# Optimization experiments

Hardware: AMD Instinct MI355X
Metric: run time of the kernel (lower is better)

Reference implementation:

```python
import jax, jax.numpy as jnp
import numpy as np

KH = KW = 3  # fixed: distortion() generates a 9-tap (3x3) offset grid


def make_offset(h, w, dilation=1.0, skydome=True):
    """Faithful numpy port of DistortionConvLayer.distortion -> [1,h,w,9,2] (last dim = [x_off, y_off])."""
    pi = np.pi
    unit_w = 2.0 * pi / w
    unit_h = pi / (2.0 * h) if skydome else pi / h
    rho = np.tan(unit_w) * dilation
    v = np.array([0.0, 1.0, 0.0])
    r_grid = np.array([[1, -1], [1, 0], [1, 1], [0, -1], [0, 0], [0, 1], [-1, -1], [-1, 0], [-1, 1]], dtype=np.float64)
    xc = int(w * 0.5)
    theta = (xc - 0.5 * w) * unit_w
    y = np.arange(h, dtype=np.float64)
    phi = (h - y) * unit_h if skydome else (h * 0.5 - y) * unit_h  # [h]
    p_u = np.stack([np.cos(phi) * np.cos(theta), np.sin(phi), np.cos(phi) * np.sin(theta)], axis=-1)  # [h,3]
    t_x = np.cross(np.broadcast_to(v, p_u.shape), p_u)  # [h,3]
    t_y = np.cross(p_u, t_x)                            # [h,3]
    # r_sphere: [h,9,3]
    r_sphere = rho * (r_grid[None, :, 0, None] * t_x[:, None, :] + r_grid[None, :, 1, None] * t_y[:, None, :])
    p_ur = p_u[:, None, :] + r_sphere  # [h,9,3]
    ux, uy, uz = p_ur[..., 0], p_ur[..., 1], p_ur[..., 2]
    base = np.arctan2(uz, ux)
    theta_r = np.where(ux > 0, base,
               np.where(ux < 0, np.where(uz >= 0, base + pi, base - pi),
                np.where(uz > 0, pi * 0.5, -pi * 0.5)))
    phi_r = np.arcsin(uy)
    x_r = (theta_r / pi + 1.0) * 0.5 * w
    y_r = (1.0 - 2.0 * phi_r / pi) * h if skydome else (0.5 - phi_r / pi) * h
    k = np.stack([x_r, y_r], axis=-1)          # [h,9,2], entries [x, y] (as in original)
    off = k - k[:, 4:5, :]                      # subtract center tap
    off = np.broadcast_to(off[:, None, :, :], (h, w, 9, 2))  # tile over width
    return off[None].astype(np.float32)         # [1,h,w,9,2]


def setup_inputs() -> dict:
    key = jax.random.key(0)
    k1, k2 = jax.random.split(key)
    B, H, W, C, F = 4, 128, 256, 64, 128
    inputs = jax.random.normal(k1, (B, H, W, C), dtype=jnp.float32)
    fan_in = KH * KW * C
    kernel = jax.random.normal(k2, (fan_in, F), dtype=jnp.float32) * (1.0 / np.sqrt(fan_in))
    bias = jnp.zeros((F,), dtype=jnp.float32)
    return {"inputs": inputs, "kernel": kernel, "bias": bias}


def reference(inputs, kernel, bias):
    B, H, W, C = inputs.shape
    F = kernel.shape[1]
    off = jnp.asarray(make_offset(H, W))  # [1,H,W,9,2], static constant
    # 'same' padding for 3x3, stride 1, dilation 1 -> pad 1 on each side
    xp = jnp.pad(inputs, ((0, 0), (1, 1), (1, 1), (0, 0)))
    in_h, in_w = H + 2, W + 2
    # base conv sampling coordinates (extract_patches order: tap k -> dy=k//3, dx=k%3)
    dy = jnp.repeat(jnp.arange(KH), KW).astype(jnp.float32)  # [9]
    dx = jnp.tile(jnp.arange(KW), KH).astype(jnp.float32)    # [9]
    base_y = jnp.arange(H, dtype=jnp.float32)[None, :, None, None] + dy[None, None, None, :]  # [1,H,1,9]
    base_x = jnp.arange(W, dtype=jnp.float32)[None, None, :, None] + dx[None, None, None, :]  # [1,1,W,9]
    # NOTE: faithful to original: channel 0 of offset (x_r diffs) is added to y, channel 1 to x
    y = base_y + off[..., 0]  # [1,H,W,9]
    x = base_x + off[..., 1]
    y = jnp.clip(y, 0.0, in_h - 1)
    x = jnp.where(x < 0, x + in_w, x)
    x = jnp.where(x > in_w - 1, x - in_w, x)
    y0 = jnp.floor(y).astype(jnp.int32)
    x0 = jnp.floor(x).astype(jnp.int32)
    y1, x1 = y0 + 1, x0 + 1
    y0 = jnp.clip(y0, 0, in_h - 1); y1 = jnp.clip(y1, 0, in_h - 1)
    x0 = jnp.clip(x0, 0, in_w - 1); x1 = jnp.clip(x1, 0, in_w - 1)
    bidx = jnp.arange(B)[:, None, None, None]  # [B,1,1,1], broadcasts against [1,H,W,9]
    gather = lambda yi, xi: xp[bidx, yi, xi]   # -> [B,H,W,9,C]
    p0 = gather(y0, x0); p1 = gather(y0, x1); p2 = gather(y1, x0); p3 = gather(y1, x1)
    y0f, y1f = y0.astype(jnp.float32), y1.astype(jnp.float32)
    x0f, x1f = x0.astype(jnp.float32), x1.astype(jnp.float32)
    w0 = ((y1f - y) * (x1f - x))[..., None]
    w1 = ((y1f - y) * (x - x0f))[..., None]
    w2 = ((y - y0f) * (x1f - x))[..., None]
    w3 = ((y - y0f) * (x - x0f))[..., None]
    pixels = w0 * p0 + w1 * p1 + w2 * p2 + w3 * p3  # [B,H,W,9,C]
    pixels = pixels.reshape(B, H * W, KH * KW * C)
    out = pixels @ kernel + bias                    # [B,HW,F]
    return jax.nn.relu(out.reshape(B, H, W, F))
```

## Files before the change

### kernel.cpp

```cpp
#include <hip/hip_runtime.h>
#include <math.h>

#define Bb 4
#define Hh 128
#define Ww 256
#define Cc 64
#define Ff 128
#define INH 130
#define INW 258

#define WSLOT 72
#define WCOLS 68

typedef __attribute__((ext_vector_type(8))) __bf16 bf16x8;
typedef __attribute__((ext_vector_type(4))) float floatx4;

__device__ __forceinline__ unsigned short f2bf(float f) {
  unsigned int u = __float_as_uint(f);
  unsigned int r = u + 0x7fffu + ((u >> 16) & 1u);
  return (unsigned short)(r >> 16);
}

__device__ __forceinline__ unsigned int cvt_pk_bf16(float lo, float hi) {
  unsigned int r;
  asm("v_cvt_pk_bf16_f32 %0, %1, %2" : "=v"(r) : "v"(lo), "v"(hi));
  return r;
}

__global__ void prep_kernel(const float* __restrict__ kmat,
                            float* __restrict__ offtab,
                            unsigned short* __restrict__ kTB) {
  int gid = blockIdx.x * 256 + threadIdx.x;
  if (gid < 576 * 128) {
    int f = gid & 127;
    int k = gid >> 7;
    int tap = k >> 6;
    int r = k & 63;
    int kk = r >> 5;
    int quad = (r >> 3) & 3;
    int i = r & 7;
    int chunk = tap * 8 + kk * 4 + quad;
    kTB[((size_t)chunk * 128 + f) * 8 + i] = f2bf(kmat[gid]);
  }
  if (gid < Hh * 9) {
    int h = gid / 9;
    int j = gid - h * 9;
    const double pi = 3.14159265358979323846;
    double unit_w = 2.0 * pi / (double)Ww;
    double unit_h = pi / (2.0 * (double)Hh);
    double rho = tan(unit_w);
    double theta = ((double)(Ww / 2) - 0.5 * (double)Ww) * unit_w;
    double phi = ((double)Hh - (double)h) * unit_h;
    double cph = cos(phi), sph = sin(phi);
    double cth = cos(theta), sth = sin(theta);
    double pux = cph * cth, puy = sph, puz = cph * sth;
    double txx = puz, txy = 0.0, txz = -pux;
    double tyx = puy * txz - puz * txy;
    double tyy = puz * txx - pux * txz;
    double tyz = pux * txy - puy * txx;
    const int r0t[9] = {1, 1, 1, 0, 0, 0, -1, -1, -1};
    const int r1t[9] = {-1, 0, 1, -1, 0, 1, -1, 0, 1};
    auto proj = [&](int r0, int r1, double& xr, double& yr) {
      double ux = pux + rho * ((double)r0 * txx + (double)r1 * tyx);
      double uy = puy + rho * ((double)r0 * txy + (double)r1 * tyy);
      double uz = puz + rho * ((double)r0 * txz + (double)r1 * tyz);
      double base = atan2(uz, ux);
      double th;
      if (ux > 0.0)        th = base;
      else if (ux < 0.0)   th = (uz >= 0.0) ? base + pi : base - pi;
      else                 th = (uz > 0.0) ? pi * 0.5 : -pi * 0.5;
      double ph = asin(uy);
      xr = (th / pi + 1.0) * 0.5 * (double)Ww;
      yr = (1.0 - 2.0 * ph / pi) * (double)Hh;
    };
    double xc, yc, xj, yj;
    proj(0, 0, xc, yc);
    proj(r0t[j], r1t[j], xj, yj);
    offtab[gid * 2 + 0] = (float)(xj - xc);
    offtab[gid * 2 + 1] = (float)(yj - yc);
  }
}

__global__ __launch_bounds__(256, 5) void fused_kernel(
    const float* __restrict__ in, const float* __restrict__ bias,
    const unsigned short* __restrict__ kTB, const float* __restrict__ offtab,
    float* __restrict__ out) {
  __shared__ unsigned short winH[2][WCOLS * WSLOT];

  int lidx = ((blockIdx.x & 7) << 8) | (blockIdx.x >> 3);
  int wt = lidx & 3;
  int h  = (lidx >> 2) & 127;
  int b  = lidx >> 9;
  int w0 = wt << 6;

  int tid  = threadIdx.x;
  int lane = tid & 63;
  int wave = tid >> 6;
  int m_base = (wave >> 1) << 5;
  int n_base = (wave & 1) << 6;
  int l15  = lane & 15;
  int quad = lane >> 4;

  floatx4 acc[2][4];
#pragma unroll
  for (int i = 0; i < 2; i++)
#pragma unroll
    for (int j = 0; j < 4; j++) acc[i][j] = (floatx4){0.f, 0.f, 0.f, 0.f};

  const float* inb = in + (size_t)b * Hh * Ww * Cc;
  const bf16x8* kbase = (const bf16x8*)kTB;

  for (int tap = 0; tap < 9; tap++) {
    float off0 = offtab[(h * 9 + tap) * 2 + 0];
    float off1 = offtab[(h * 9 + tap) * 2 + 1];
    float dyk = (float)(tap / 3), dxk = (float)(tap % 3);

    float y = (float)h + dyk + off0;
    y = fminf(fmaxf(y, 0.f), (float)(INH - 1));
    int y0i = (int)floorf(y);
    int y1i = y0i + 1;
    y0i = min(max(y0i, 0), INH - 1);
    y1i = min(max(y1i, 0), INH - 1);
    float wy0 = (float)y1i - y;
    float wy1 = y - (float)y0i;
    if (!(y0i >= 1 && y0i <= Hh)) wy0 = 0.f;
    if (!(y1i >= 1 && y1i <= Hh)) wy1 = 0.f;
    const float* row0 = inb + (size_t)min(max(y0i - 1, 0), Hh - 1) * Ww * Cc;
    const float* row1 = inb + (size_t)min(max(y1i - 1, 0), Hh - 1) * Ww * Cc;

    float xrep = (float)w0 + dxk + off1;
    float flo  = floorf(xrep);
    int jb = (int)flo - 1;
    float fr = xrep - flo;
    float q00 = wy0 * (1.f - fr), q01 = wy0 * fr;
    float q10 = wy1 * (1.f - fr), q11 = wy1 * fr;

    int slotv[2];
#pragma unroll
    for (int mi = 0; mi < 2; mi++) {
      int w = m_base + mi * 16 + l15;
      float x = (float)(w0 + w) + dxk + off1;
      if (x < 0.f) x += (float)INW;
      if (x > (float)(INW - 1)) x -= (float)INW;
      int x0i = (int)floorf(x);
      int s = x0i - jb;
      if (s < 0) s += INW;
      if (s > WCOLS - 1) s = WCOLS - 1;
      slotv[mi] = s;
    }

    unsigned short* win = winH[tap & 1];
    const char* r0 = (const char*)row0;
    const char* r1 = (const char*)row1;

    for (int it = 0; it < 3; it++) {
      int task = tid + (it << 8);
      if (task < WCOLS * 8) {
        int j  = task >> 3;
        int c8 = (task & 7) << 3;
        int col = jb + j;
        if (col < 0) col += INW;
        if (col > INW - 1) col -= INW;
        int ncol = (col == INW - 1) ? 0 : col + 1;
        bool jok = (j < WCOLS - 1);
        bool cok = ((unsigned)(col - 1) < (unsigned)Ww) & jok;
        bool nok = ((unsigned)(ncol - 1) < (unsigned)Ww) & jok;
        unsigned offc = (((unsigned)((col - 1) & (Ww - 1))) << 8) + ((unsigned)c8 << 2);
        unsigned offn = (((unsigned)((ncol - 1) & (Ww - 1))) << 8) + ((unsigned)c8 << 2);
        float w00 = cok ? q00 : 0.f;
        float w01 = nok ? q01 : 0.f;
        float w10 = cok ? q10 : 0.f;
        float w11 = nok ? q11 : 0.f;
        uint4 st;
        {
          float4 a0 = *(const float4*)(r0 + offc);
          float4 a1 = *(const float4*)(r0 + offn);
          float4 b0 = *(const float4*)(r1 + offc);
          float4 b1 = *(const float4*)(r1 + offn);
          float px = w00 * a0.x + w01 * a1.x + w10 * b0.x + w11 * b1.x;
          float py = w00 * a0.y + w01 * a1.y + w10 * b0.y + w11 * b1.y;
          float pz = w00 * a0.z + w01 * a1.z + w10 * b0.z + w11 * b1.z;
          float pw = w00 * a0.w + w01 * a1.w + w10 * b0.w + w11 * b1.w;
          st.x = cvt_pk_bf16(px, py);
          st.y = cvt_pk_bf16(pz, pw);
        }
        {
          float4 a0 = *(const float4*)(r0 + offc + 16);
          float4 a1 = *(const float4*)(r0 + offn + 16);
          float4 b0 = *(const float4*)(r1 + offc + 16);
          float4 b1 = *(const float4*)(r1 + offn + 16);
          float px = w00 * a0.x + w01 * a1.x + w10 * b0.x + w11 * b1.x;
          float py = w00 * a0.y + w01 * a1.y + w10 * b0.y + w11 * b1.y;
          float pz = w00 * a0.z + w01 * a1.z + w10 * b0.z + w11 * b1.z;
          float pw = w00 * a0.w + w01 * a1.w + w10 * b0.w + w11 * b1.w;
          st.z = cvt_pk_bf16(px, py);
          st.w = cvt_pk_bf16(pz, pw);
        }
        *(uint4*)(&win[j * WSLOT + c8]) = st;
      }
    }

    int ch0 = (tap * 8 + quad) * 128;
    bf16x8 bfrag0[4];
#pragma unroll
    for (int v = 0; v < 4; v++)
      bfrag0[v] = kbase[ch0 + n_base + v * 16 + l15];

    __syncthreads();

    bf16x8 af[2];
#pragma unroll
    for (int mi = 0; mi < 2; mi++)
      af[mi] = *(const bf16x8*)&win[slotv[mi] * WSLOT + quad * 8];
    bf16x8 bfrag1[4];
#pragma unroll
    for (int v = 0; v < 4; v++)
      bfrag1[v] = kbase[ch0 + 4 * 128 + n_base + v * 16 + l15];
#pragma unroll
    for (int mi = 0; mi < 2; mi++)
#pragma unroll
      for (int v = 0; v < 4; v++)
        acc[mi][v] = __builtin_amdgcn_mfma_f32_16x16x32_bf16(
            af[mi], bfrag0[v], acc[mi][v], 0, 0, 0);
#pragma unroll
    for (int mi = 0; mi < 2; mi++)
      af[mi] = *(const bf16x8*)&win[slotv[mi] * WSLOT + 32 + quad * 8];
#pragma unroll
    for (int mi = 0; mi < 2; mi++)
#pragma unroll
      for (int v = 0; v < 4; v++)
        acc[mi][v] = __builtin_amdgcn_mfma_f32_16x16x32_bf16(
            af[mi], bfrag1[v], acc[mi][v], 0, 0, 0);
  }

  size_t outbase = ((size_t)(b * Hh + h) * Ww + w0);
#pragma unroll
  for (int ni = 0; ni < 4; ni++) {
    int f = n_base + ni * 16 + l15;
    float bv = bias[f];
#pragma unroll
    for (int mi = 0; mi < 2; mi++) {
#pragma unroll
      for (int r = 0; r < 4; r++) {
        int m = m_base + mi * 16 + quad * 4 + r;
        out[(outbase + m) * Ff + f] = fmaxf(acc[mi][ni][r] + bv, 0.f);
      }
    }
  }
}

extern "C" void kernel_launch(void* const* d_in, const int* in_sizes, int n_in,
                              void* d_out, int out_size, void* d_ws, size_t ws_size,
                              hipStream_t stream) {
  const float* in   = (const float*)d_in[0];
  const float* kmat = (const float*)d_in[1];
  const float* bias = (const float*)d_in[2];
  float* out = (float*)d_out;

  float* offtab = (float*)d_ws;
  unsigned short* kTB = (unsigned short*)((char*)d_ws + Hh * 9 * 2 * sizeof(float));
  if (ws_size < (size_t)(Hh * 9 * 2 * sizeof(float) + 128 * 576 * sizeof(unsigned short)))
    return;

  prep_kernel<<<288, 256, 0, stream>>>(kmat, offtab, kTB);
  fused_kernel<<<Bb * Hh * (Ww / 64), 256, 0, stream>>>(in, bias, kTB, offtab, out);
}
```

Measured before the change: 152.9 us.

## Give each wave a private sampling window and drop block-wide barriers

Each block now covers 128 output columns instead of 64. Each wave builds its own 36-column bilinear-sampled bf16 window in its own slice of shared memory and computes all 128 output channels for its 32 columns. This removes the __syncthreads per tap and the redundant window rows shared across waves, and halves the grid. In exchange each wave holds twice as many accumulators, occupancy drops (launch bounds 5 to 3), and sample positions that fall outside a wave's local window are clamped to a zeroed dummy slot, which assumes the offsets stay within that range.

```diff
diff --git a/kernel.cpp b/kernel.cpp
--- a/kernel.cpp
+++ b/kernel.cpp
@@ -10,7 +10,7 @@
 #define INW 258
 
 #define WSLOT 72
-#define WCOLS 68
+#define WPW 37
 
 typedef __attribute__((ext_vector_type(8))) __bf16 bf16x8;
 typedef __attribute__((ext_vector_type(4))) float floatx4;
@@ -81,31 +81,33 @@
   }
 }
 
-__global__ __launch_bounds__(256, 5) void fused_kernel(
+__global__ __launch_bounds__(256, 3) void fused_kernel(
     const float* __restrict__ in, const float* __restrict__ bias,
     const unsigned short* __restrict__ kTB, const float* __restrict__ offtab,
     float* __restrict__ out) {
-  __shared__ unsigned short winH[2][WCOLS * WSLOT];
-
-  int lidx = ((blockIdx.x & 7) << 8) | (blockIdx.x >> 3);
-  int wt = lidx & 3;
-  int h  = (lidx >> 2) & 127;
-  int b  = lidx >> 9;
-  int w0 = wt << 6;
+  __shared__ unsigned short winH[4 * WPW * WSLOT];
+
+  int lidx = ((blockIdx.x & 7) << 7) | (blockIdx.x >> 3);
+  int wt = lidx & 1;
+  int h  = (lidx >> 1) & 127;
+  int b  = lidx >> 8;
+  int w0 = wt << 7;
 
   int tid  = threadIdx.x;
   int lane = tid & 63;
   int wave = tid >> 6;
-  int m_base = (wave >> 1) << 5;
-  int n_base = (wave & 1) << 6;
+  int m_base = wave << 5;
   int l15  = lane & 15;
   int quad = lane >> 4;
 
-  floatx4 acc[2][4];
+  unsigned short* win = &winH[wave * (WPW * WSLOT)];
+  if (lane < 18) *(uint2*)&win[36 * WSLOT + lane * 4] = (uint2){0u, 0u};
+
+  floatx4 acc[2][8];
 #pragma unroll
   for (int i = 0; i < 2; i++)
 #pragma unroll
-    for (int j = 0; j < 4; j++) acc[i][j] = (floatx4){0.f, 0.f, 0.f, 0.f};
+    for (int j = 0; j < 8; j++) acc[i][j] = (floatx4){0.f, 0.f, 0.f, 0.f};
 
   const float* inb = in + (size_t)b * Hh * Ww * Cc;
   const bf16x8* kbase = (const bf16x8*)kTB;
@@ -125,8 +127,8 @@
     float wy1 = y - (float)y0i;
     if (!(y0i >= 1 && y0i <= Hh)) wy0 = 0.f;
     if (!(y1i >= 1 && y1i <= Hh)) wy1 = 0.f;
-    const float* row0 = inb + (size_t)min(max(y0i - 1, 0), Hh - 1) * Ww * Cc;
-    const float* row1 = inb + (size_t)min(max(y1i - 1, 0), Hh - 1) * Ww * Cc;
+    const char* r0 = (const char*)(inb + (size_t)min(max(y0i - 1, 0), Hh - 1) * Ww * Cc);
+    const char* r1 = (const char*)(inb + (size_t)min(max(y1i - 1, 0), Hh - 1) * Ww * Cc);
 
     float xrep = (float)w0 + dxk + off1;
     float flo  = floorf(xrep);
@@ -138,33 +140,29 @@
     int slotv[2];
 #pragma unroll
     for (int mi = 0; mi < 2; mi++) {
-      int w = m_base + mi * 16 + l15;
-      float x = (float)(w0 + w) + dxk + off1;
+      int wr = m_base + mi * 16 + l15;
+      float x = (float)(w0 + wr) + dxk + off1;
       if (x < 0.f) x += (float)INW;
       if (x > (float)(INW - 1)) x -= (float)INW;
       int x0i = (int)floorf(x);
       int s = x0i - jb;
       if (s < 0) s += INW;
-      if (s > WCOLS - 1) s = WCOLS - 1;
-      slotv[mi] = s;
-    }
-
-    unsigned short* win = winH[tap & 1];
-    const char* r0 = (const char*)row0;
-    const char* r1 = (const char*)row1;
-
-    for (int it = 0; it < 3; it++) {
-      int task = tid + (it << 8);
-      if (task < WCOLS * 8) {
-        int j  = task >> 3;
-        int c8 = (task & 7) << 3;
-        int col = jb + j;
+      int ls = s - m_base;
+      if ((unsigned)ls > 35u) ls = 36;
+      slotv[mi] = ls;
+    }
+
+    for (int it = 0; it < 5; it++) {
+      int t = lane + (it << 6);
+      if (t < 36 * 8) {
+        int ls = t >> 3;
+        int c8 = (t & 7) << 3;
+        int col = jb + m_base + ls;
         if (col < 0) col += INW;
         if (col > INW - 1) col -= INW;
         int ncol = (col == INW - 1) ? 0 : col + 1;
-        bool jok = (j < WCOLS - 1);
-        bool cok = ((unsigned)(col - 1) < (unsigned)Ww) & jok;
-        bool nok = ((unsigned)(ncol - 1) < (unsigned)Ww) & jok;
+        bool cok = ((unsigned)(col - 1) < (unsigned)Ww);
+        bool nok = ((unsigned)(ncol - 1) < (unsigned)Ww);
         unsigned offc = (((unsigned)((col - 1) & (Ww - 1))) << 8) + ((unsigned)c8 << 2);
         unsigned offn = (((unsigned)((ncol - 1) & (Ww - 1))) << 8) + ((unsigned)c8 << 2);
         float w00 = cok ? q00 : 0.f;
@@ -196,47 +194,28 @@
           st.z = cvt_pk_bf16(px, py);
           st.w = cvt_pk_bf16(pz, pw);
         }
-        *(uint4*)(&win[j * WSLOT + c8]) = st;
+        *(uint4*)(&win[ls * WSLOT + c8]) = st;
       }
     }
 
-    int ch0 = (tap * 8 + quad) * 128;
-    bf16x8 bfrag0[4];
-#pragma unroll
-    for (int v = 0; v < 4; v++)
-      bfrag0[v] = kbase[ch0 + n_base + v * 16 + l15];
-
-    __syncthreads();
-
-    bf16x8 af[2];
-#pragma unroll
-    for (int mi = 0; mi < 2; mi++)
-      af[mi] = *(const bf16x8*)&win[slotv[mi] * WSLOT + quad * 8];
-    bf16x8 bfrag1[4];
-#pragma unroll
-    for (int v = 0; v < 4; v++)
-      bfrag1[v] = kbase[ch0 + 4 * 128 + n_base + v * 16 + l15];
-#pragma unroll
-    for (int mi = 0; mi < 2; mi++)
-#pragma unroll
-      for (int v = 0; v < 4; v++)
-        acc[mi][v] = __builtin_amdgcn_mfma_f32_16x16x32_bf16(
-            af[mi], bfrag0[v], acc[mi][v], 0, 0, 0);
-#pragma unroll
-    for (int mi = 0; mi < 2; mi++)
-      af[mi] = *(const bf16x8*)&win[slotv[mi] * WSLOT + 32 + quad * 8];
-#pragma unroll
-    for (int mi = 0; mi < 2; mi++)
-#pragma unroll
-      for (int v = 0; v < 4; v++)
-        acc[mi][v] = __builtin_amdgcn_mfma_f32_16x16x32_bf16(
-            af[mi], bfrag1[v], acc[mi][v], 0, 0, 0);
+#pragma unroll
+    for (int kk = 0; kk < 2; kk++) {
+      int ch0 = (tap * 8 + kk * 4 + quad) * 128;
+      bf16x8 af0 = *(const bf16x8*)&win[slotv[0] * WSLOT + kk * 32 + quad * 8];
+      bf16x8 af1 = *(const bf16x8*)&win[slotv[1] * WSLOT + kk * 32 + quad * 8];
+#pragma unroll
+      for (int ni = 0; ni < 8; ni++) {
+        bf16x8 bf = kbase[ch0 + ni * 16 + l15];
+        acc[0][ni] = __builtin_amdgcn_mfma_f32_16x16x32_bf16(af0, bf, acc[0][ni], 0, 0, 0);
+        acc[1][ni] = __builtin_amdgcn_mfma_f32_16x16x32_bf16(af1, bf, acc[1][ni], 0, 0, 0);
+      }
+    }
   }
 
   size_t outbase = ((size_t)(b * Hh + h) * Ww + w0);
 #pragma unroll
-  for (int ni = 0; ni < 4; ni++) {
-    int f = n_base + ni * 16 + l15;
+  for (int ni = 0; ni < 8; ni++) {
+    int f = ni * 16 + l15;
     float bv = bias[f];
 #pragma unroll
     for (int mi = 0; mi < 2; mi++) {
@@ -263,5 +242,5 @@
     return;
 
   prep_kernel<<<288, 256, 0, stream>>>(kmat, offtab, kTB);
-  fused_kernel<<<Bb * Hh * (Ww / 64), 256, 0, stream>>>(in, bias, kTB, offtab, out);
-}
+  fused_kernel<<<Bb * Hh * (Ww / 128), 256, 0, stream>>>(in, bias, kTB, offtab, out);
+}
```

After: 156.5 us. 2.3% more time.
